# Kernel tuning notes

Hardware: AMD Instinct MI355X
Metric: run time of the kernel (lower is better)

## Reference

```python
import jax, jax.numpy as jnp
import numpy as np

N, E, L, H = 40000, 120000, 6, 128
DIN, DEDGE, DOUT = 11, 3, 3
EPS = 1e-5


def _mlp_ln(h, w1, b1, w2, b2, g, b):
    # Linear -> ReLU -> Linear -> LayerNorm
    h = jax.nn.relu(h @ w1 + b1) @ w2 + b2
    mu = jnp.mean(h, axis=-1, keepdims=True)
    var = jnp.var(h, axis=-1, keepdims=True)
    return (h - mu) * jax.lax.rsqrt(var + EPS) * g + b


def setup_inputs() -> dict:
    key = jax.random.key(0)
    ks = iter(jax.random.split(key, 64))

    def W(shape):
        fan_in = shape[-2]
        return jax.random.normal(next(ks), shape, jnp.float32) / np.sqrt(fan_in)

    inp = {
        'x': jax.random.normal(next(ks), (N, DIN), jnp.float32),
        'edge_attr': jax.random.normal(next(ks), (E, DEDGE), jnp.float32),
        'edge_index': jax.random.randint(next(ks), (2, E), 0, N, dtype=jnp.int64),
        'mean_x': jax.random.normal(next(ks), (DIN,), jnp.float32),
        'std_x': jnp.ones((DIN,), jnp.float32),
        'mean_edge': jax.random.normal(next(ks), (DEDGE,), jnp.float32),
        'std_edge': jnp.ones((DEDGE,), jnp.float32),
        # node / edge encoders
        'en_w1': W((DIN, H)), 'en_b1': jnp.zeros((H,)), 'en_w2': W((H, H)), 'en_b2': jnp.zeros((H,)),
        'en_g': jnp.ones((H,)), 'en_b': jnp.zeros((H,)),
        'ee_w1': W((DEDGE, H)), 'ee_b1': jnp.zeros((H,)), 'ee_w2': W((H, H)), 'ee_b2': jnp.zeros((H,)),
        'ee_g': jnp.ones((H,)), 'ee_b': jnp.zeros((H,)),
        # processor blocks, stacked over L layers
        'pn_w1': W((L, 2 * H, H)), 'pn_b1': jnp.zeros((L, H)), 'pn_w2': W((L, H, H)), 'pn_b2': jnp.zeros((L, H)),
        'pn_g': jnp.ones((L, H)), 'pn_b': jnp.zeros((L, H)),
        'pe_w1': W((L, 3 * H, H)), 'pe_b1': jnp.zeros((L, H)), 'pe_w2': W((L, H, H)), 'pe_b2': jnp.zeros((L, H)),
        'pe_g': jnp.ones((L, H)), 'pe_b': jnp.zeros((L, H)),
        # decoder
        'dec_w1': W((H, H)), 'dec_b1': jnp.zeros((H,)), 'dec_w2': W((H, DOUT)), 'dec_b2': jnp.zeros((DOUT,)),
    }
    return inp


def reference(x, edge_attr, edge_index, mean_x, std_x, mean_edge, std_edge,
              en_w1, en_b1, en_w2, en_b2, en_g, en_b,
              ee_w1, ee_b1, ee_w2, ee_b2, ee_g, ee_b,
              pn_w1, pn_b1, pn_w2, pn_b2, pn_g, pn_b,
              pe_w1, pe_b1, pe_w2, pe_b2, pe_g, pe_b,
              dec_w1, dec_b1, dec_w2, dec_b2):
    # input normalization + encoders
    x = (x - mean_x) / std_x
    ea = (edge_attr - mean_edge) / std_edge
    x = _mlp_ln(x, en_w1, en_b1, en_w2, en_b2, en_g, en_b)          # [N, H]
    ea = _mlp_ln(ea, ee_w1, ee_b1, ee_w2, ee_b2, ee_g, ee_b)        # [E, H]

    src = edge_index[0]  # j (source); also aggregation index in the original
    dst = edge_index[1]  # i (target)

    def step(carry, p):
        x, ea = carry
        nw1, nb1, nw2, nb2, ng, nb, ew1, eb1, ew2, eb2, eg, eb = p
        # message: MLP(cat[x_i, x_j, edge_attr]) + edge_attr
        m = _mlp_ln(jnp.concatenate([x[dst], x[src], ea], axis=1),
                    ew1, eb1, ew2, eb2, eg, eb) + ea                # [E, H]
        # aggregate (index_add_ at edge_index[0], as in the source)
        agg = jax.ops.segment_sum(m, src, num_segments=N)            # [N, H]
        # node update with residual
        x = x + _mlp_ln(jnp.concatenate([x, agg], axis=1),
                        nw1, nb1, nw2, nb2, ng, nb)
        return (x, m), None

    (x, ea), _ = jax.lax.scan(
        step, (x, ea),
        (pn_w1, pn_b1, pn_w2, pn_b2, pn_g, pn_b,
         pe_w1, pe_b1, pe_w2, pe_b2, pe_g, pe_b))

    return jax.nn.relu(x @ dec_w1 + dec_b1) @ dec_w2 + dec_b2       # [N, DOUT]
```

## Files before the change

kernel.cpp:

```cpp
#include <hip/hip_runtime.h>
#include <hip/hip_bf16.h>

#define HH 128
#define LAYERS 6
#define EPS_LN 1e-5f
#define NN 40000
#define EE 120000

typedef short vs8  __attribute__((ext_vector_type(8)));
typedef float f32x4 __attribute__((ext_vector_type(4)));

__device__ __forceinline__ short f2b(float f){ __hip_bfloat16 h=__float2bfloat16(f); short s; __builtin_memcpy(&s,&h,2); return s; }
__device__ __forceinline__ float b2f(short s){ __hip_bfloat16 h; __builtin_memcpy(&h,&s,2); return __bfloat162float(h); }
__device__ __forceinline__ float cvf(const void* p, size_t i, int f32){
    return f32 ? ((const float*)p)[i] : __bfloat162float(((const __hip_bfloat16*)p)[i]);
}

__device__ __forceinline__ void stage16(short* dst, const short* src, int tid){
    ((int4*)dst)[tid]       = ((const int4*)src)[tid];
    ((int4*)dst)[tid + 256] = ((const int4*)src)[tid + 256];
}

struct PtrTab { const void* p[35]; };

#define VO_EN_B1 0
#define VO_EN_B2 128
#define VO_EN_G  256
#define VO_EN_B  384
#define VO_EE_B1 512
#define VO_EE_B2 640
#define VO_EE_G  768
#define VO_EE_B  896
#define VO_PE_B1 1024
#define VO_PE_B2 1792
#define VO_PE_G  2560
#define VO_PE_B  3328
#define VO_PN_B1 4096
#define VO_PN_B2 4864
#define VO_PN_G  5632
#define VO_PN_B  6400
#define VO_DEC_B1 7168
#define VO_DEC_B2 7296
#define VO_DEC_W2 7424
#define VO_MEAN_X 7808
#define VO_STD_X  7824
#define VO_MEAN_E 7840
#define VO_STD_E  7856
#define VO_EN_W1  7872
#define VO_EE_W1  9280

__global__ void detect_kernel(PtrTab P, int* __restrict__ flags)
{
    if (threadIdx.x == 0 && blockIdx.x == 0) {
        flags[0] = (((const unsigned*)P.p[4])[0] == 0x3F800000u) ? 1 : 0;
        const unsigned* e = (const unsigned*)P.p[2];
        unsigned acc = 0;
        for (int k = 0; k < 32; ++k) acc |= e[2 * k + 1];
        flags[1] = (acc == 0u) ? 1 : 0;
    }
}

__device__ void cpv(float* vws, int off, const void* src, int n, int f, int t)
{
    for (int i = t; i < n; i += 256) vws[off + i] = cvf(src, i, f);
}

__global__ void prep_misc(PtrTab P, float* __restrict__ vws,
                          int* __restrict__ srcv, int* __restrict__ dstv,
                          int* __restrict__ cnt, const int* __restrict__ flags)
{
    const int t = threadIdx.x, f = flags[0];
    if (blockIdx.x == 0) {
        cpv(vws, VO_EN_B1, P.p[8],  128, f, t);  cpv(vws, VO_EN_B2, P.p[10], 128, f, t);
        cpv(vws, VO_EN_G,  P.p[11], 128, f, t);  cpv(vws, VO_EN_B,  P.p[12], 128, f, t);
        cpv(vws, VO_EE_B1, P.p[14], 128, f, t);  cpv(vws, VO_EE_B2, P.p[16], 128, f, t);
        cpv(vws, VO_EE_G,  P.p[17], 128, f, t);  cpv(vws, VO_EE_B,  P.p[18], 128, f, t);
        cpv(vws, VO_PE_B1, P.p[26], 768, f, t);  cpv(vws, VO_PE_B2, P.p[28], 768, f, t);
        cpv(vws, VO_PE_G,  P.p[29], 768, f, t);  cpv(vws, VO_PE_B,  P.p[30], 768, f, t);
        cpv(vws, VO_PN_B1, P.p[20], 768, f, t);  cpv(vws, VO_PN_B2, P.p[22], 768, f, t);
        cpv(vws, VO_PN_G,  P.p[23], 768, f, t);  cpv(vws, VO_PN_B,  P.p[24], 768, f, t);
        cpv(vws, VO_DEC_B1, P.p[32], 128, f, t); cpv(vws, VO_DEC_B2, P.p[34], 3, f, t);
        cpv(vws, VO_DEC_W2, P.p[33], 384, f, t);
        cpv(vws, VO_MEAN_X, P.p[3], 11, f, t);   cpv(vws, VO_STD_X, P.p[4], 11, f, t);
        cpv(vws, VO_MEAN_E, P.p[5], 3, f, t);    cpv(vws, VO_STD_E, P.p[6], 3, f, t);
        cpv(vws, VO_EN_W1, P.p[7], 11 * 128, f, t);
        cpv(vws, VO_EE_W1, P.p[13], 3 * 128, f, t);
    }
    const int e = blockIdx.x * 256 + t;
    if (e < EE) {
        int s, d;
        if (flags[1]) {
            const long long* p = (const long long*)P.p[2];
            s = (int)p[e]; d = (int)p[(size_t)EE + e];
        } else {
            const int* p = (const int*)P.p[2];
            s = p[e]; d = p[EE + e];
        }
        srcv[e] = s; dstv[e] = d;
        atomicAdd(&cnt[s], 1);
    }
}

struct WDesc { const void* src; short* dst; int K; int base; int size; };
struct WTab  { WDesc d[7]; };

__global__ void pack_w_all(WTab T, const int* __restrict__ flags)
{
    const int id = blockIdx.x * 256 + threadIdx.x;
    int s = -1;
    #pragma unroll
    for (int k = 0; k < 7; ++k)
        if (id >= T.d[k].base && id < T.d[k].base + T.d[k].size) s = k;
    if (s < 0) return;
    const int K = T.d[s].K, nk = K >> 5;
    const int local = id - T.d[s].base;
    const int lane = local & 63;
    const int r    = local >> 6;
    const int ct   = r & 7;
    const int r2   = r >> 3;
    const int kk   = r2 % nk;
    const int m    = r2 / nk;
    const int f    = flags[0];
    const size_t so = (size_t)m * K * HH + ((size_t)(kk * 32 + (lane >> 4) * 8)) * HH
                    + ct * 16 + (lane & 15);
    const size_t dof = (size_t)local * 8;
    #pragma unroll
    for (int j = 0; j < 8; ++j)
        T.d[s].dst[dof + j] = f2b(cvf(T.d[s].src, so + (size_t)j * HH, f));
}

__global__ void scan_block(const int* __restrict__ cnt, int* __restrict__ startv,
                           int* __restrict__ bsum, int N)
{
    __shared__ int sh[256];
    const int b = blockIdx.x, t = threadIdx.x, n = b * 256 + t;
    int v = (n < N) ? cnt[n] : 0;
    sh[t] = v; __syncthreads();
    for (int o = 1; o < 256; o <<= 1) {
        int x = (t >= o) ? sh[t - o] : 0; __syncthreads();
        sh[t] += x; __syncthreads();
    }
    if (n < N) startv[n] = sh[t] - v;
    if (t == 255) bsum[b] = sh[t];
}

__global__ void scan_top(int* __restrict__ bsum, int NB)
{
    __shared__ int sh[256];
    const int t = threadIdx.x;
    int v = (t < NB) ? bsum[t] : 0;
    sh[t] = v; __syncthreads();
    for (int o = 1; o < 256; o <<= 1) {
        int x = (t >= o) ? sh[t - o] : 0; __syncthreads();
        sh[t] += x; __syncthreads();
    }
    if (t < NB) bsum[t] = sh[t] - v;
}

__global__ void scan_add(int* __restrict__ startv, const int* __restrict__ bsum,
                         int* __restrict__ cursor, int N)
{
    const int n = blockIdx.x * 256 + threadIdx.x;
    if (n >= N) return;
    const int s = startv[n] + bsum[n >> 8];
    startv[n] = s; cursor[n] = s;
}

__global__ void scatter_kernel(const int* __restrict__ srcv, const int* __restrict__ dstv,
                               int* __restrict__ cursor, int* __restrict__ eorder,
                               int* __restrict__ srcs, int* __restrict__ dsts, int E)
{
    const int e = blockIdx.x * 256 + threadIdx.x;
    if (e >= E) return;
    const int s = srcv[e];
    const int p = atomicAdd(&cursor[s], 1);
    eorder[p] = e;
    srcs[p] = s;
    dsts[p] = dstv[e];
}

__launch_bounds__(256, 4)
__global__ void edge_mfma(const short* __restrict__ x, short* __restrict__ ea,
                          const int* __restrict__ srcs, const int* __restrict__ dsts,
                          const short* __restrict__ w1p, const short* __restrict__ w2p,
                          const float* __restrict__ bias1, const float* __restrict__ bias2,
                          const float* __restrict__ gammaf, const float* __restrict__ betaf)
{
    const int tid = threadIdx.x, wave = tid >> 6, lane = tid & 63;
    const int q = lane >> 4, lm = lane & 15;
    const int e0 = blockIdx.x * 64;
    const int myrow = e0 + wave * 16 + lm;
    __shared__ __align__(16) short wbuf[2][4096];
    __shared__ __align__(16) short H_s[64][136];

    const short* xd = x + (size_t)dsts[myrow] * HH;
    const short* xs = x + (size_t)srcs[myrow] * HH;
    const short* er = ea + (size_t)myrow * HH;

    vs8 afr[12];
    #pragma unroll
    for (int kk = 0; kk < 4; ++kk) {
        afr[kk]     = *(const vs8*)(xd + kk * 32 + q * 8);
        afr[4 + kk] = *(const vs8*)(xs + kk * 32 + q * 8);
        afr[8 + kk] = *(const vs8*)(er + kk * 32 + q * 8);
    }

    stage16(wbuf[0], w1p, tid);
    __syncthreads();

    f32x4 acc[8];
    #pragma unroll
    for (int c = 0; c < 8; ++c) acc[c] = (f32x4)0.f;

    #pragma unroll
    for (int kk = 0; kk < 12; ++kk) {
        const int p = kk & 1;
        if (kk < 11) stage16(wbuf[1 - p], w1p + (size_t)(kk + 1) * 4096, tid);
        else         stage16(wbuf[1 - p], w2p, tid);
        #pragma unroll
        for (int c = 0; c < 8; ++c) {
            vs8 b = *(const vs8*)&wbuf[p][(c * 64 + lane) * 8];
            acc[c] = __builtin_amdgcn_mfma_f32_16x16x32_bf16(afr[kk], b, acc[c], 0, 0, 0);
        }
        __syncthreads();
    }

    float b1v[8], b2v[8], gv[8], bv[8];
    #pragma unroll
    for (int c = 0; c < 8; ++c) {
        const int col = c * 16 + lm;
        b1v[c] = bias1[col]; b2v[c] = bias2[col]; gv[c] = gammaf[col]; bv[c] = betaf[col];
    }

    #pragma unroll
    for (int c = 0; c < 8; ++c) {
        const int col = c * 16 + lm;
        #pragma unroll
        for (int reg = 0; reg < 4; ++reg)
            H_s[wave * 16 + q * 4 + reg][col] = f2b(fmaxf(acc[c][reg] + b1v[c], 0.f));
    }

    f32x4 acc2[8];
    #pragma unroll
    for (int c = 0; c < 8; ++c) acc2[c] = (f32x4)0.f;
    #pragma unroll
    for (int j = 0; j < 4; ++j) {
        const int p = j & 1;
        if (j < 3) stage16(wbuf[1 - p], w2p + (size_t)(j + 1) * 4096, tid);
        vs8 a = *(const vs8*)&H_s[wave * 16 + lm][j * 32 + q * 8];
        #pragma unroll
        for (int c = 0; c < 8; ++c) {
            vs8 b = *(const vs8*)&wbuf[p][(c * 64 + lane) * 8];
            acc2[c] = __builtin_amdgcn_mfma_f32_16x16x32_bf16(a, b, acc2[c], 0, 0, 0);
        }
        if (j < 3) __syncthreads();
    }

    #pragma unroll
    for (int reg = 0; reg < 4; ++reg) {
        float vv[8], s = 0.f, s2 = 0.f;
        #pragma unroll
        for (int c = 0; c < 8; ++c) {
            float v = acc2[c][reg] + b2v[c];
            vv[c] = v; s += v; s2 += v * v;
        }
        #pragma unroll
        for (int off = 1; off < 16; off <<= 1) { s += __shfl_xor(s, off); s2 += __shfl_xor(s2, off); }
        const float mu = s * (1.f / 128.f);
        const float rs = rsqrtf(s2 * (1.f / 128.f) - mu * mu + EPS_LN);
        #pragma unroll
        for (int c = 0; c < 8; ++c)
            H_s[wave * 16 + q * 4 + reg][c * 16 + lm] = f2b((vv[c] - mu) * rs * gv[c] + bv[c]);
    }

    {
        short* ew = ea + (size_t)myrow * HH;
        #pragma unroll
        for (int kk = 0; kk < 4; ++kk) {
            vs8 nv = *(const vs8*)&H_s[wave * 16 + lm][kk * 32 + q * 8];
            union { vs8 v; short el[8]; } u;
            #pragma unroll
            for (int j = 0; j < 8; ++j)
                u.el[j] = f2b(b2f(nv[j]) + b2f(afr[8 + kk][j]));
            *(vs8*)(ew + kk * 32 + q * 8) = u.v;
        }
    }
}

__launch_bounds__(256, 4)
__global__ void node_mfma(short* __restrict__ x, const short* __restrict__ m,
                          const int* __restrict__ startv, const int* __restrict__ cnt,
                          const short* __restrict__ w1p, const short* __restrict__ w2p,
                          const float* __restrict__ bias1, const float* __restrict__ bias2,
                          const float* __restrict__ gammaf, const float* __restrict__ betaf)
{
    const int tid = threadIdx.x, wave = tid >> 6, lane = tid & 63;
    const int q = lane >> 4, lm = lane & 15;
    const int n0 = blockIdx.x * 64;
    const int myrow = n0 + wave * 16 + lm;
    __shared__ __align__(16) short wbuf[2][4096];
    __shared__ __align__(16) short H_s[64][136];

    const short* xr = x + (size_t)myrow * HH;
    const int s0 = startv[myrow], c0 = cnt[myrow];

    vs8 afr[8];
    #pragma unroll
    for (int kk = 0; kk < 4; ++kk)
        afr[kk] = *(const vs8*)(xr + kk * 32 + q * 8);
    {
        float af[4][8];
        #pragma unroll
        for (int kk = 0; kk < 4; ++kk)
            #pragma unroll
            for (int j = 0; j < 8; ++j) af[kk][j] = 0.f;
        for (int i = 0; i < c0; ++i) {
            const short* mr = m + (size_t)(s0 + i) * HH;
            #pragma unroll
            for (int kk = 0; kk < 4; ++kk) {
                vs8 v = *(const vs8*)(mr + kk * 32 + q * 8);
                #pragma unroll
                for (int j = 0; j < 8; ++j) af[kk][j] += b2f(v[j]);
            }
        }
        #pragma unroll
        for (int kk = 0; kk < 4; ++kk) {
            union { vs8 v; short el[8]; } u;
            #pragma unroll
            for (int j = 0; j < 8; ++j) u.el[j] = f2b(af[kk][j]);
            afr[4 + kk] = u.v;
        }
    }

    stage16(wbuf[0], w1p, tid);
    __syncthreads();

    f32x4 acc[8];
    #pragma unroll
    for (int c = 0; c < 8; ++c) acc[c] = (f32x4)0.f;

    #pragma unroll
    for (int kk = 0; kk < 8; ++kk) {
        const int p = kk & 1;
        if (kk < 7) stage16(wbuf[1 - p], w1p + (size_t)(kk + 1) * 4096, tid);
        else        stage16(wbuf[1 - p], w2p, tid);
        #pragma unroll
        for (int c = 0; c < 8; ++c) {
            vs8 b = *(const vs8*)&wbuf[p][(c * 64 + lane) * 8];
            acc[c] = __builtin_amdgcn_mfma_f32_16x16x32_bf16(afr[kk], b, acc[c], 0, 0, 0);
        }
        __syncthreads();
    }

    float b1v[8], b2v[8], gv[8], bv[8];
    #pragma unroll
    for (int c = 0; c < 8; ++c) {
        const int col = c * 16 + lm;
        b1v[c] = bias1[col]; b2v[c] = bias2[col]; gv[c] = gammaf[col]; bv[c] = betaf[col];
    }

    #pragma unroll
    for (int c = 0; c < 8; ++c) {
        const int col = c * 16 + lm;
        #pragma unroll
        for (int reg = 0; reg < 4; ++reg)
            H_s[wave * 16 + q * 4 + reg][col] = f2b(fmaxf(acc[c][reg] + b1v[c], 0.f));
    }

    f32x4 acc2[8];
    #pragma unroll
    for (int c = 0; c < 8; ++c) acc2[c] = (f32x4)0.f;
    #pragma unroll
    for (int j = 0; j < 4; ++j) {
        const int p = j & 1;
        if (j < 3) stage16(wbuf[1 - p], w2p + (size_t)(j + 1) * 4096, tid);
        vs8 a = *(const vs8*)&H_s[wave * 16 + lm][j * 32 + q * 8];
        #pragma unroll
        for (int c = 0; c < 8; ++c) {
            vs8 b = *(const vs8*)&wbuf[p][(c * 64 + lane) * 8];
            acc2[c] = __builtin_amdgcn_mfma_f32_16x16x32_bf16(a, b, acc2[c], 0, 0, 0);
        }
        if (j < 3) __syncthreads();
    }

    #pragma unroll
    for (int reg = 0; reg < 4; ++reg) {
        float vv[8], s = 0.f, s2 = 0.f;
        #pragma unroll
        for (int c = 0; c < 8; ++c) {
            float v = acc2[c][reg] + b2v[c];
            vv[c] = v; s += v; s2 += v * v;
        }
        #pragma unroll
        for (int off = 1; off < 16; off <<= 1) { s += __shfl_xor(s, off); s2 += __shfl_xor(s2, off); }
        const float mu = s * (1.f / 128.f);
        const float rs = rsqrtf(s2 * (1.f / 128.f) - mu * mu + EPS_LN);
        #pragma unroll
        for (int c = 0; c < 8; ++c)
            H_s[wave * 16 + q * 4 + reg][c * 16 + lm] = f2b((vv[c] - mu) * rs * gv[c] + bv[c]);
    }

    {
        short* xw = x + (size_t)myrow * HH;
        #pragma unroll
        for (int kk = 0; kk < 4; ++kk) {
            vs8 nv = *(const vs8*)&H_s[wave * 16 + lm][kk * 32 + q * 8];
            union { vs8 v; short el[8]; } u;
            #pragma unroll
            for (int j = 0; j < 8; ++j)
                u.el[j] = f2b(b2f(nv[j]) + b2f(afr[kk][j]));
            *(vs8*)(xw + kk * 32 + q * 8) = u.v;
        }
    }
}

template<int K, int KP>
__launch_bounds__(256, 4)
__global__ void enc_mfma(const void* __restrict__ in,
                         const float* __restrict__ meanv, const float* __restrict__ stdv,
                         const float* __restrict__ w1f, const float* __restrict__ bias1,
                         const short* __restrict__ w2p, const float* __restrict__ bias2,
                         const float* __restrict__ gammaf, const float* __restrict__ betaf,
                         short* __restrict__ out, const int* __restrict__ flags,
                         const int* __restrict__ perm)
{
    const int tid = threadIdx.x, wave = tid >> 6, lane = tid & 63;
    const int q = lane >> 4, lm = lane & 15;
    const int r0 = blockIdx.x * 64;
    __shared__ float xn_s[64][KP];
    __shared__ __align__(16) short wbuf[2][4096];
    __shared__ __align__(16) short H_s[64][136];

    const int f = flags[0];
    for (int i = tid; i < 64 * KP; i += 256) {
        const int r = i / KP, k = i % KP;
        if (k < K) {
            const int rr = perm ? perm[r0 + r] : (r0 + r);
            xn_s[r][k] = (cvf(in, (size_t)rr * K + k, f) - meanv[k]) / stdv[k];
        }
    }
    __syncthreads();

    for (int i = tid; i < 64 * HH; i += 256) {
        const int r = i >> 7, c = i & 127;
        float a = bias1[c];
        #pragma unroll
        for (int k = 0; k < K; ++k) a += xn_s[r][k] * w1f[k * HH + c];
        H_s[r][c] = f2b(fmaxf(a, 0.f));
    }
    stage16(wbuf[0], w2p, tid);
    __syncthreads();

    f32x4 acc2[8];
    #pragma unroll
    for (int c = 0; c < 8; ++c) acc2[c] = (f32x4)0.f;
    #pragma unroll
    for (int j = 0; j < 4; ++j) {
        const int p = j & 1;
        if (j < 3) stage16(wbuf[1 - p], w2p + (size_t)(j + 1) * 4096, tid);
        vs8 a = *(const vs8*)&H_s[wave * 16 + lm][j * 32 + q * 8];
        #pragma unroll
        for (int c = 0; c < 8; ++c) {
            vs8 b = *(const vs8*)&wbuf[p][(c * 64 + lane) * 8];
            acc2[c] = __builtin_amdgcn_mfma_f32_16x16x32_bf16(a, b, acc2[c], 0, 0, 0);
        }
        __syncthreads();
    }
    float b2v[8], gv[8], bv[8];
    #pragma unroll
    for (int c = 0; c < 8; ++c) {
        const int col = c * 16 + lm;
        b2v[c] = bias2[col]; gv[c] = gammaf[col]; bv[c] = betaf[col];
    }
    #pragma unroll
    for (int reg = 0; reg < 4; ++reg) {
        float s = 0.f, s2 = 0.f;
        #pragma unroll
        for (int c = 0; c < 8; ++c) {
            float v = acc2[c][reg] + b2v[c];
            acc2[c][reg] = v; s += v; s2 += v * v;
        }
        #pragma unroll
        for (int off = 1; off < 16; off <<= 1) { s += __shfl_xor(s, off); s2 += __shfl_xor(s2, off); }
        const float mu = s * (1.f / 128.f);
        const float rs = rsqrtf(s2 * (1.f / 128.f) - mu * mu + EPS_LN);
        const int row = r0 + wave * 16 + q * 4 + reg;
        #pragma unroll
        for (int c = 0; c < 8; ++c) {
            const int col = c * 16 + lm;
            out[(size_t)row * HH + col] = f2b((acc2[c][reg] - mu) * rs * gv[c] + bv[c]);
        }
    }
}

__launch_bounds__(256)
__global__ void dec_mfma(const short* __restrict__ x, const short* __restrict__ w1p,
                         const float* __restrict__ bias1, const float* __restrict__ w2f,
                         const float* __restrict__ b2f3, void* __restrict__ out,
                         const int* __restrict__ flags)
{
    const int tid = threadIdx.x, wave = tid >> 6, lane = tid & 63;
    const int q = lane >> 4, lm = lane & 15;
    const int r0 = blockIdx.x * 64;
    const int myrow = r0 + wave * 16 + lm;
    __shared__ __align__(16) short H_s[64][136];

    f32x4 acc[8];
    #pragma unroll
    for (int c = 0; c < 8; ++c) acc[c] = (f32x4)0.f;
    #pragma unroll
    for (int kk = 0; kk < 4; ++kk) {
        vs8 a = *(const vs8*)(x + (size_t)myrow * HH + kk * 32 + q * 8);
        const short* bp = w1p + ((size_t)(kk * 8) * 64 + lane) * 8;
        #pragma unroll
        for (int c = 0; c < 8; ++c) {
            vs8 b = *(const vs8*)(bp + (size_t)c * 64 * 8);
            acc[c] = __builtin_amdgcn_mfma_f32_16x16x32_bf16(a, b, acc[c], 0, 0, 0);
        }
    }
    #pragma unroll
    for (int c = 0; c < 8; ++c) {
        const int col = c * 16 + lm;
        const float bb1 = bias1[col];
        #pragma unroll
        for (int reg = 0; reg < 4; ++reg)
            H_s[wave * 16 + q * 4 + reg][col] = f2b(fmaxf(acc[c][reg] + bb1, 0.f));
    }
    __syncthreads();

    if (tid < 192) {
        const int r = tid / 3, o = tid - 3 * r;
        float a = b2f3[o];
        #pragma unroll 8
        for (int k = 0; k < HH; ++k) a += b2f(H_s[r][k]) * w2f[k * 3 + o];
        const size_t oi = (size_t)(r0 + r) * 3 + o;
        if (flags[0]) ((float*)out)[oi] = a;
        else ((__hip_bfloat16*)out)[oi] = __float2bfloat16(a);
    }
}

extern "C" void kernel_launch(void* const* d_in, const int* in_sizes, int n_in,
                              void* d_out, int out_size, void* d_ws, size_t ws_size,
                              hipStream_t stream)
{
    char* base = (char*)d_ws;
    size_t off = 0;
    auto alloc = [&](size_t bytes) { void* r = base + off; off = (off + bytes + 255) & ~(size_t)255; return r; };

    int*   flags  = (int*)alloc(256);
    int*   srcv   = (int*)alloc((size_t)EE * 4);
    int*   dstv   = (int*)alloc((size_t)EE * 4);
    int*   srcs   = (int*)alloc((size_t)EE * 4);
    int*   dsts   = (int*)alloc((size_t)EE * 4);
    short* xb     = (short*)alloc((size_t)NN * HH * 2);
    short* eab    = (short*)alloc((size_t)EE * HH * 2);
    float* vws    = (float*)alloc(16384 * 4);
    short* pe_w1p = (short*)alloc((size_t)6 * 384 * HH * 2);
    short* pe_w2p = (short*)alloc((size_t)6 * HH * HH * 2);
    short* pn_w1p = (short*)alloc((size_t)6 * 256 * HH * 2);
    short* pn_w2p = (short*)alloc((size_t)6 * HH * HH * 2);
    short* en_w2p = (short*)alloc((size_t)HH * HH * 2);
    short* ee_w2p = (short*)alloc((size_t)HH * HH * 2);
    short* dc_w1p = (short*)alloc((size_t)HH * HH * 2);
    int*   cnt    = (int*)alloc((size_t)NN * 4);
    int*   startv = (int*)alloc((size_t)NN * 4);
    int*   cursor = (int*)alloc((size_t)NN * 4);
    int*   eorder = (int*)alloc((size_t)EE * 4);
    int*   bsum   = (int*)alloc(1024);

    PtrTab P;
    for (int i = 0; i < 35; ++i) P.p[i] = d_in[i];

    detect_kernel<<<1, 64, 0, stream>>>(P, flags);
    (void)hipMemsetAsync(cnt, 0, (size_t)NN * 4, stream);
    prep_misc<<<(EE + 255) / 256, 256, 0, stream>>>(P, vws, srcv, dstv, cnt, flags);

    WTab T;
    int b = 0;
    auto seg = [&](int i, const void* src, short* dst, int K, int nmat) {
        int sz = nmat * (K / 32) * 512;
        T.d[i] = WDesc{src, dst, K, b, sz};
        b += sz;
    };
    seg(0, d_in[25], pe_w1p, 384, 6);
    seg(1, d_in[27], pe_w2p, 128, 6);
    seg(2, d_in[19], pn_w1p, 256, 6);
    seg(3, d_in[21], pn_w2p, 128, 6);
    seg(4, d_in[9],  en_w2p, 128, 1);
    seg(5, d_in[15], ee_w2p, 128, 1);
    seg(6, d_in[31], dc_w1p, 128, 1);
    pack_w_all<<<(b + 255) / 256, 256, 0, stream>>>(T, flags);

    const int NB = (NN + 255) / 256;
    scan_block<<<NB, 256, 0, stream>>>(cnt, startv, bsum, NN);
    scan_top<<<1, 256, 0, stream>>>(bsum, NB);
    scan_add<<<NB, 256, 0, stream>>>(startv, bsum, cursor, NN);
    scatter_kernel<<<(EE + 255) / 256, 256, 0, stream>>>(srcv, dstv, cursor,
                                                         eorder, srcs, dsts, EE);

    enc_mfma<11, 16><<<NN / 64, 256, 0, stream>>>(d_in[0],
        vws + VO_MEAN_X, vws + VO_STD_X, vws + VO_EN_W1, vws + VO_EN_B1,
        en_w2p, vws + VO_EN_B2, vws + VO_EN_G, vws + VO_EN_B, xb, flags, nullptr);
    enc_mfma<3, 4><<<EE / 64, 256, 0, stream>>>(d_in[1],
        vws + VO_MEAN_E, vws + VO_STD_E, vws + VO_EE_W1, vws + VO_EE_B1,
        ee_w2p, vws + VO_EE_B2, vws + VO_EE_G, vws + VO_EE_B, eab, flags, eorder);

    for (int l = 0; l < LAYERS; ++l) {
        edge_mfma<<<EE / 64, 256, 0, stream>>>(xb, eab, srcs, dsts,
            pe_w1p + (size_t)l * 384 * HH, pe_w2p + (size_t)l * HH * HH,
            vws + VO_PE_B1 + l * HH, vws + VO_PE_B2 + l * HH,
            vws + VO_PE_G + l * HH, vws + VO_PE_B + l * HH);
        node_mfma<<<NN / 64, 256, 0, stream>>>(xb, eab, startv, cnt,
            pn_w1p + (size_t)l * 256 * HH, pn_w2p + (size_t)l * HH * HH,
            vws + VO_PN_B1 + l * HH, vws + VO_PN_B2 + l * HH,
            vws + VO_PN_G + l * HH, vws + VO_PN_B + l * HH);
    }

    dec_mfma<<<NN / 64, 256, 0, stream>>>(xb, dc_w1p, vws + VO_DEC_B1,
        vws + VO_DEC_W2, vws + VO_DEC_B2, d_out, flags);
}
```

Baseline: 610.3 us.

## Stage weights in 32-row chunks and write outputs as coalesced tile stores

The edge, node and encoder MLP kernels now double-buffer weight slices covering two K-steps at a time, which halves the number of barriers in the GEMM loops. The shared weight buffer doubles in size, so the occupancy hint drops from 4 to 3 blocks per CU. Final outputs are first assembled in shared memory and then written as fully coalesced 16-byte stores per block, replacing the per-lane scattered row writes. The encoder also issues its weight prefetch earlier so it overlaps the first-layer compute. The cost is more LDS per block, lower occupancy and extra syncs on the output path.

```diff
diff --git a/kernel.cpp b/kernel.cpp
--- a/kernel.cpp
+++ b/kernel.cpp
@@ -16,9 +16,10 @@
     return f32 ? ((const float*)p)[i] : __bfloat162float(((const __hip_bfloat16*)p)[i]);
 }
 
-__device__ __forceinline__ void stage16(short* dst, const short* src, int tid){
-    ((int4*)dst)[tid]       = ((const int4*)src)[tid];
-    ((int4*)dst)[tid + 256] = ((const int4*)src)[tid + 256];
+__device__ __forceinline__ void stage32(short* dst, const short* src, int tid){
+    #pragma unroll
+    for (int i = 0; i < 4; ++i)
+        ((int4*)dst)[tid + i * 256] = ((const int4*)src)[tid + i * 256];
 }
 
 struct PtrTab { const void* p[35]; };
@@ -179,7 +180,7 @@
     dsts[p] = dstv[e];
 }
 
-__launch_bounds__(256, 4)
+__launch_bounds__(256, 3)
 __global__ void edge_mfma(const short* __restrict__ x, short* __restrict__ ea,
                           const int* __restrict__ srcs, const int* __restrict__ dsts,
                           const short* __restrict__ w1p, const short* __restrict__ w2p,
@@ -190,7 +191,7 @@
     const int q = lane >> 4, lm = lane & 15;
     const int e0 = blockIdx.x * 64;
     const int myrow = e0 + wave * 16 + lm;
-    __shared__ __align__(16) short wbuf[2][4096];
+    __shared__ __align__(16) short wbuf[2][8192];
     __shared__ __align__(16) short H_s[64][136];
 
     const short* xd = x + (size_t)dsts[myrow] * HH;
@@ -205,7 +206,7 @@
         afr[8 + kk] = *(const vs8*)(er + kk * 32 + q * 8);
     }
 
-    stage16(wbuf[0], w1p, tid);
+    stage32(wbuf[0], w1p, tid);
     __syncthreads();
 
     f32x4 acc[8];
@@ -213,14 +214,17 @@
     for (int c = 0; c < 8; ++c) acc[c] = (f32x4)0.f;
 
     #pragma unroll
-    for (int kk = 0; kk < 12; ++kk) {
-        const int p = kk & 1;
-        if (kk < 11) stage16(wbuf[1 - p], w1p + (size_t)(kk + 1) * 4096, tid);
-        else         stage16(wbuf[1 - p], w2p, tid);
-        #pragma unroll
-        for (int c = 0; c < 8; ++c) {
-            vs8 b = *(const vs8*)&wbuf[p][(c * 64 + lane) * 8];
-            acc[c] = __builtin_amdgcn_mfma_f32_16x16x32_bf16(afr[kk], b, acc[c], 0, 0, 0);
+    for (int s = 0; s < 6; ++s) {
+        const int p = s & 1;
+        if (s < 5) stage32(wbuf[1 - p], w1p + (size_t)(s + 1) * 8192, tid);
+        else       stage32(wbuf[1 - p], w2p, tid);
+        #pragma unroll
+        for (int k2 = 0; k2 < 2; ++k2) {
+            #pragma unroll
+            for (int c = 0; c < 8; ++c) {
+                vs8 b = *(const vs8*)&wbuf[p][k2 * 4096 + (c * 64 + lane) * 8];
+                acc[c] = __builtin_amdgcn_mfma_f32_16x16x32_bf16(afr[s * 2 + k2], b, acc[c], 0, 0, 0);
+            }
         }
         __syncthreads();
     }
@@ -244,16 +248,19 @@
     #pragma unroll
     for (int c = 0; c < 8; ++c) acc2[c] = (f32x4)0.f;
     #pragma unroll
-    for (int j = 0; j < 4; ++j) {
+    for (int j = 0; j < 2; ++j) {
         const int p = j & 1;
-        if (j < 3) stage16(wbuf[1 - p], w2p + (size_t)(j + 1) * 4096, tid);
-        vs8 a = *(const vs8*)&H_s[wave * 16 + lm][j * 32 + q * 8];
-        #pragma unroll
-        for (int c = 0; c < 8; ++c) {
-            vs8 b = *(const vs8*)&wbuf[p][(c * 64 + lane) * 8];
-            acc2[c] = __builtin_amdgcn_mfma_f32_16x16x32_bf16(a, b, acc2[c], 0, 0, 0);
-        }
-        if (j < 3) __syncthreads();
+        if (j < 1) stage32(wbuf[1 - p], w2p + 8192, tid);
+        #pragma unroll
+        for (int k2 = 0; k2 < 2; ++k2) {
+            vs8 a = *(const vs8*)&H_s[wave * 16 + lm][(j * 2 + k2) * 32 + q * 8];
+            #pragma unroll
+            for (int c = 0; c < 8; ++c) {
+                vs8 b = *(const vs8*)&wbuf[p][k2 * 4096 + (c * 64 + lane) * 8];
+                acc2[c] = __builtin_amdgcn_mfma_f32_16x16x32_bf16(a, b, acc2[c], 0, 0, 0);
+            }
+        }
+        if (j < 1) __syncthreads();
     }
 
     #pragma unroll
@@ -273,21 +280,27 @@
             H_s[wave * 16 + q * 4 + reg][c * 16 + lm] = f2b((vv[c] - mu) * rs * gv[c] + bv[c]);
     }
 
+    #pragma unroll
+    for (int kk = 0; kk < 4; ++kk) {
+        vs8 nv = *(const vs8*)&H_s[wave * 16 + lm][kk * 32 + q * 8];
+        union { vs8 v; short el[8]; } u;
+        #pragma unroll
+        for (int j = 0; j < 8; ++j)
+            u.el[j] = f2b(b2f(nv[j]) + b2f(afr[8 + kk][j]));
+        *(vs8*)&H_s[wave * 16 + lm][kk * 32 + q * 8] = u.v;
+    }
+    __syncthreads();
     {
-        short* ew = ea + (size_t)myrow * HH;
-        #pragma unroll
-        for (int kk = 0; kk < 4; ++kk) {
-            vs8 nv = *(const vs8*)&H_s[wave * 16 + lm][kk * 32 + q * 8];
-            union { vs8 v; short el[8]; } u;
-            #pragma unroll
-            for (int j = 0; j < 8; ++j)
-                u.el[j] = f2b(b2f(nv[j]) + b2f(afr[8 + kk][j]));
-            *(vs8*)(ew + kk * 32 + q * 8) = u.v;
-        }
-    }
-}
-
-__launch_bounds__(256, 4)
+        int4* g = (int4*)(ea + (size_t)e0 * HH);
+        #pragma unroll
+        for (int it = 0; it < 4; ++it) {
+            const int i = tid + it * 256;
+            g[i] = *(const int4*)&H_s[i >> 4][(i & 15) * 8];
+        }
+    }
+}
+
+__launch_bounds__(256, 3)
 __global__ void node_mfma(short* __restrict__ x, const short* __restrict__ m,
                           const int* __restrict__ startv, const int* __restrict__ cnt,
                           const short* __restrict__ w1p, const short* __restrict__ w2p,
@@ -298,7 +311,7 @@
     const int q = lane >> 4, lm = lane & 15;
     const int n0 = blockIdx.x * 64;
     const int myrow = n0 + wave * 16 + lm;
-    __shared__ __align__(16) short wbuf[2][4096];
+    __shared__ __align__(16) short wbuf[2][8192];
     __shared__ __align__(16) short H_s[64][136];
 
     const short* xr = x + (size_t)myrow * HH;
@@ -332,7 +345,7 @@
         }
     }
 
-    stage16(wbuf[0], w1p, tid);
+    stage32(wbuf[0], w1p, tid);
     __syncthreads();
 
     f32x4 acc[8];
@@ -340,14 +353,17 @@
     for (int c = 0; c < 8; ++c) acc[c] = (f32x4)0.f;
 
     #pragma unroll
-    for (int kk = 0; kk < 8; ++kk) {
-        const int p = kk & 1;
-        if (kk < 7) stage16(wbuf[1 - p], w1p + (size_t)(kk + 1) * 4096, tid);
-        else        stage16(wbuf[1 - p], w2p, tid);
-        #pragma unroll
-        for (int c = 0; c < 8; ++c) {
-            vs8 b = *(const vs8*)&wbuf[p][(c * 64 + lane) * 8];
-            acc[c] = __builtin_amdgcn_mfma_f32_16x16x32_bf16(afr[kk], b, acc[c], 0, 0, 0);
+    for (int s = 0; s < 4; ++s) {
+        const int p = s & 1;
+        if (s < 3) stage32(wbuf[1 - p], w1p + (size_t)(s + 1) * 8192, tid);
+        else       stage32(wbuf[1 - p], w2p, tid);
+        #pragma unroll
+        for (int k2 = 0; k2 < 2; ++k2) {
+            #pragma unroll
+            for (int c = 0; c < 8; ++c) {
+                vs8 b = *(const vs8*)&wbuf[p][k2 * 4096 + (c * 64 + lane) * 8];
+                acc[c] = __builtin_amdgcn_mfma_f32_16x16x32_bf16(afr[s * 2 + k2], b, acc[c], 0, 0, 0);
+            }
         }
         __syncthreads();
     }
@@ -371,16 +387,19 @@
     #pragma unroll
     for (int c = 0; c < 8; ++c) acc2[c] = (f32x4)0.f;
     #pragma unroll
-    for (int j = 0; j < 4; ++j) {
+    for (int j = 0; j < 2; ++j) {
         const int p = j & 1;
-        if (j < 3) stage16(wbuf[1 - p], w2p + (size_t)(j + 1) * 4096, tid);
-        vs8 a = *(const vs8*)&H_s[wave * 16 + lm][j * 32 + q * 8];
-        #pragma unroll
-        for (int c = 0; c < 8; ++c) {
-            vs8 b = *(const vs8*)&wbuf[p][(c * 64 + lane) * 8];
-            acc2[c] = __builtin_amdgcn_mfma_f32_16x16x32_bf16(a, b, acc2[c], 0, 0, 0);
-        }
-        if (j < 3) __syncthreads();
+        if (j < 1) stage32(wbuf[1 - p], w2p + 8192, tid);
+        #pragma unroll
+        for (int k2 = 0; k2 < 2; ++k2) {
+            vs8 a = *(const vs8*)&H_s[wave * 16 + lm][(j * 2 + k2) * 32 + q * 8];
+            #pragma unroll
+            for (int c = 0; c < 8; ++c) {
+                vs8 b = *(const vs8*)&wbuf[p][k2 * 4096 + (c * 64 + lane) * 8];
+                acc2[c] = __builtin_amdgcn_mfma_f32_16x16x32_bf16(a, b, acc2[c], 0, 0, 0);
+            }
+        }
+        if (j < 1) __syncthreads();
     }
 
     #pragma unroll
@@ -400,22 +419,28 @@
             H_s[wave * 16 + q * 4 + reg][c * 16 + lm] = f2b((vv[c] - mu) * rs * gv[c] + bv[c]);
     }
 
+    #pragma unroll
+    for (int kk = 0; kk < 4; ++kk) {
+        vs8 nv = *(const vs8*)&H_s[wave * 16 + lm][kk * 32 + q * 8];
+        union { vs8 v; short el[8]; } u;
+        #pragma unroll
+        for (int j = 0; j < 8; ++j)
+            u.el[j] = f2b(b2f(nv[j]) + b2f(afr[kk][j]));
+        *(vs8*)&H_s[wave * 16 + lm][kk * 32 + q * 8] = u.v;
+    }
+    __syncthreads();
     {
-        short* xw = x + (size_t)myrow * HH;
-        #pragma unroll
-        for (int kk = 0; kk < 4; ++kk) {
-            vs8 nv = *(const vs8*)&H_s[wave * 16 + lm][kk * 32 + q * 8];
-            union { vs8 v; short el[8]; } u;
-            #pragma unroll
-            for (int j = 0; j < 8; ++j)
-                u.el[j] = f2b(b2f(nv[j]) + b2f(afr[kk][j]));
-            *(vs8*)(xw + kk * 32 + q * 8) = u.v;
+        int4* g = (int4*)(x + (size_t)n0 * HH);
+        #pragma unroll
+        for (int it = 0; it < 4; ++it) {
+            const int i = tid + it * 256;
+            g[i] = *(const int4*)&H_s[i >> 4][(i & 15) * 8];
         }
     }
 }
 
 template<int K, int KP>
-__launch_bounds__(256, 4)
+__launch_bounds__(256, 3)
 __global__ void enc_mfma(const void* __restrict__ in,
                          const float* __restrict__ meanv, const float* __restrict__ stdv,
                          const float* __restrict__ w1f, const float* __restrict__ bias1,
@@ -428,7 +453,7 @@
     const int q = lane >> 4, lm = lane & 15;
     const int r0 = blockIdx.x * 64;
     __shared__ float xn_s[64][KP];
-    __shared__ __align__(16) short wbuf[2][4096];
+    __shared__ __align__(16) short wbuf[2][8192];
     __shared__ __align__(16) short H_s[64][136];
 
     const int f = flags[0];
@@ -439,6 +464,7 @@
             xn_s[r][k] = (cvf(in, (size_t)rr * K + k, f) - meanv[k]) / stdv[k];
         }
     }
+    stage32(wbuf[0], w2p, tid);
     __syncthreads();
 
     for (int i = tid; i < 64 * HH; i += 256) {
@@ -448,23 +474,25 @@
         for (int k = 0; k < K; ++k) a += xn_s[r][k] * w1f[k * HH + c];
         H_s[r][c] = f2b(fmaxf(a, 0.f));
     }
-    stage16(wbuf[0], w2p, tid);
     __syncthreads();
 
     f32x4 acc2[8];
     #pragma unroll
     for (int c = 0; c < 8; ++c) acc2[c] = (f32x4)0.f;
     #pragma unroll
-    for (int j = 0; j < 4; ++j) {
+    for (int j = 0; j < 2; ++j) {
         const int p = j & 1;
-        if (j < 3) stage16(wbuf[1 - p], w2p + (size_t)(j + 1) * 4096, tid);
-        vs8 a = *(const vs8*)&H_s[wave * 16 + lm][j * 32 + q * 8];
-        #pragma unroll
-        for (int c = 0; c < 8; ++c) {
-            vs8 b = *(const vs8*)&wbuf[p][(c * 64 + lane) * 8];
-            acc2[c] = __builtin_amdgcn_mfma_f32_16x16x32_bf16(a, b, acc2[c], 0, 0, 0);
-        }
-        __syncthreads();
+        if (j < 1) stage32(wbuf[1 - p], w2p + 8192, tid);
+        #pragma unroll
+        for (int k2 = 0; k2 < 2; ++k2) {
+            vs8 a = *(const vs8*)&H_s[wave * 16 + lm][(j * 2 + k2) * 32 + q * 8];
+            #pragma unroll
+            for (int c = 0; c < 8; ++c) {
+                vs8 b = *(const vs8*)&wbuf[p][k2 * 4096 + (c * 64 + lane) * 8];
+                acc2[c] = __builtin_amdgcn_mfma_f32_16x16x32_bf16(a, b, acc2[c], 0, 0, 0);
+            }
+        }
+        if (j < 1) __syncthreads();
     }
     float b2v[8], gv[8], bv[8];
     #pragma unroll
@@ -472,23 +500,30 @@
         const int col = c * 16 + lm;
         b2v[c] = bias2[col]; gv[c] = gammaf[col]; bv[c] = betaf[col];
     }
+    __syncthreads();
     #pragma unroll
     for (int reg = 0; reg < 4; ++reg) {
-        float s = 0.f, s2 = 0.f;
+        float vv[8], s = 0.f, s2 = 0.f;
         #pragma unroll
         for (int c = 0; c < 8; ++c) {
             float v = acc2[c][reg] + b2v[c];
-            acc2[c][reg] = v; s += v; s2 += v * v;
+            vv[c] = v; s += v; s2 += v * v;
         }
         #pragma unroll
         for (int off = 1; off < 16; off <<= 1) { s += __shfl_xor(s, off); s2 += __shfl_xor(s2, off); }
         const float mu = s * (1.f / 128.f);
         const float rs = rsqrtf(s2 * (1.f / 128.f) - mu * mu + EPS_LN);
-        const int row = r0 + wave * 16 + q * 4 + reg;
-        #pragma unroll
-        for (int c = 0; c < 8; ++c) {
-            const int col = c * 16 + lm;
-            out[(size_t)row * HH + col] = f2b((acc2[c][reg] - mu) * rs * gv[c] + bv[c]);
+        #pragma unroll
+        for (int c = 0; c < 8; ++c)
+            H_s[wave * 16 + q * 4 + reg][c * 16 + lm] = f2b((vv[c] - mu) * rs * gv[c] + bv[c]);
+    }
+    __syncthreads();
+    {
+        int4* g = (int4*)(out + (size_t)r0 * HH);
+        #pragma unroll
+        for (int it = 0; it < 4; ++it) {
+            const int i = tid + it * 256;
+            g[i] = *(const int4*)&H_s[i >> 4][(i & 15) * 8];
         }
     }
 }
```

After: 552.9 us. -9.4%, faster.
